# Optimization experiments

Measured on AMD Instinct MI355X. Metric: run time of the kernel, lower is better.

Reference implementation:

```python
import jax, jax.numpy as jnp
import numpy as np

DELTA = 1.0 / 1024.0  # init kwarg `delta`


def _lin_init(key, out_f, in_f):
    k1, k2 = jax.random.split(key)
    s = 1.0 / np.sqrt(in_f)
    w = jax.random.uniform(k1, (out_f, in_f), minval=-s, maxval=s, dtype=jnp.float32)
    b = jax.random.uniform(k2, (out_f,), minval=-s, maxval=s, dtype=jnp.float32)
    return w, b


def setup_inputs() -> dict:
    key = jax.random.key(0)
    B, S, C, H, T = 262144, 64, 8, 64, 1024  # batch, state_dim, control_dim, rnn hidden, seq len
    ks = jax.random.split(key, 12)
    t = jax.random.uniform(ks[0], (B, 1), dtype=jnp.float32)            # in [0,1) -> t_u in [0,T)
    x = jax.random.normal(ks[1], (B, S), dtype=jnp.float32)
    u = jax.random.normal(ks[2], (T, C), dtype=jnp.float32)
    i2h_w, i2h_b = _lin_init(ks[3], H, C + H)
    h2o_w, h2o_b = _lin_init(ks[4], S, C + H)
    xw1, xb1 = _lin_init(ks[5], 20, 1 + S)
    xw2, xb2 = _lin_init(ks[6], 20, 20)
    xw3, xb3 = _lin_init(ks[7], S, 20)
    uw1, ub1 = _lin_init(ks[8], 20, 1 + S)
    uw2, ub2 = _lin_init(ks[9], 20, 20)
    uw3, ub3 = _lin_init(ks[10], S, 20)
    cw, cb = _lin_init(ks[11], S, 2 * S)
    return {"t": t, "x": x, "u": u,
            "i2h_w": i2h_w, "i2h_b": i2h_b, "h2o_w": h2o_w, "h2o_b": h2o_b,
            "xw1": xw1, "xb1": xb1, "xw2": xw2, "xb2": xb2, "xw3": xw3, "xb3": xb3,
            "uw1": uw1, "ub1": ub1, "uw2": uw2, "ub2": ub2, "uw3": uw3, "ub3": ub3,
            "cw": cw, "cb": cb}


def _mlp(z, w1, b1, w2, b2, w3, b3):
    h = jax.nn.sigmoid(z @ w1.T + b1)
    h = jax.nn.sigmoid(h @ w2.T + b2)
    return h @ w3.T + b3


def reference(t, x, u, i2h_w, i2h_b, h2o_w, h2o_b,
              xw1, xb1, xw2, xb2, xw3, xb3,
              uw1, ub1, uw2, ub2, uw3, ub3, cw, cb):
    # state branch: x_dnn([t, x])
    state_part = _mlp(jnp.concatenate([t, x], axis=1), xw1, xb1, xw2, xb2, xw3, xb3)

    # sequential tanh-RNN over the control sequence (hidden starts at zero)
    hsz = i2h_w.shape[0]

    def step(h, u_k):
        j = jnp.concatenate([u_k, h])                 # (C+H,)
        h_new = jnp.tanh(j @ i2h_w.T + i2h_b)         # (H,)
        out = jnp.tanh(j @ h2o_w.T + h2o_b)           # (S,)
        return h_new, out

    h0 = jnp.zeros((hsz,), dtype=u.dtype)
    _, u_rnn_out = jax.lax.scan(step, h0, u)          # (T, S)

    # gather encoded controls per query time
    t_u = jnp.floor(t / DELTA).astype(jnp.int32).squeeze(-1)  # (B,)
    encoded_controls = u_rnn_out[t_u]                 # (B, S)

    control_part = _mlp(jnp.concatenate([t, encoded_controls], axis=1),
                        uw1, ub1, uw2, ub2, uw3, ub3)

    stacked = jax.nn.sigmoid(jnp.concatenate([state_part, control_part], axis=1))  # (B, 2S)
    return stacked @ cw.T + cb
```

## Files before the change

kernel.cpp:

```cpp
#include <hip/hip_runtime.h>
#include <hip/hip_bf16.h>

#define T_SEQ 1024
#define CHUNK 64
#define NCHUNK 16

__device__ __forceinline__ float fast_sigmoid(float x) {
    return 1.0f / (1.0f + __expf(-x));
}
__device__ __forceinline__ float fast_tanh(float x) {
    float e = __expf(2.0f * x);
    return 1.0f - 2.0f / (e + 1.0f);
}

__device__ __forceinline__ float quad_sum(float x) {
    int y1 = __builtin_amdgcn_mov_dpp(__float_as_int(x), 0xB1, 0xF, 0xF, true);
    float s1 = x + __int_as_float(y1);
    int y2 = __builtin_amdgcn_mov_dpp(__float_as_int(s1), 0x4E, 0xF, 0xF, true);
    return s1 + __int_as_float(y2);
}

#define P_SW1 0
#define P_SB1 1360
#define P_SW2 1380
#define P_SB2 1780
#define P_UW1 1800
#define P_UB1 3160
#define P_UW2 3180
#define P_UB2 3580
#define P_XW3 3600
#define P_XB3 4880
#define P_UW3 4944
#define P_UB3 6224
#define P_CWT 6288
#define P_CB  14480
#define P_TOT 14544

__global__ __launch_bounds__(256) void k_prep(
    const float* __restrict__ u,
    const float* __restrict__ i2h_w, const float* __restrict__ i2h_b,
    const float* __restrict__ h2o_w, const float* __restrict__ h2o_b,
    const float* __restrict__ xw1, const float* __restrict__ uw1,
    const float* __restrict__ xw2, const float* __restrict__ uw2,
    const float* __restrict__ xw3, const float* __restrict__ uw3,
    const float* __restrict__ cw,
    const float* __restrict__ xb1, const float* __restrict__ xb2,
    const float* __restrict__ ub1, const float* __restrict__ ub2,
    const float* __restrict__ xb3, const float* __restrict__ ub3,
    const float* __restrict__ cb,
    float* __restrict__ pre_t, float* __restrict__ pre_o,
    float* __restrict__ wp) {
    const int bid = blockIdx.x, tid = threadIdx.x;
    if (bid < 256) {
        int idx = bid * 256 + tid;
        int k = idx >> 6, i = idx & 63;
        float a = i2h_b[i], b = h2o_b[i];
#pragma unroll
        for (int c = 0; c < 8; ++c) {
            float uv = u[k * 8 + c];
            a += uv * i2h_w[i * 72 + c];
            b += uv * h2o_w[i * 72 + c];
        }
        pre_t[i * 1024 + k] = a;
        pre_o[idx] = b;
        return;
    }
    int i = (bid - 256) * 256 + tid;
    if (i >= P_TOT) return;
    float v = 0.0f;
    if (i < 1360) {
        int o = i / 68, c = i - o * 68;
        if (c == 0) v = xw1[o * 65];
        else if (c >= 4) v = xw1[o * 65 + c - 3];
    } else if (i < 1380) v = xb1[i - 1360];
    else if (i < 1780) v = xw2[i - 1380];
    else if (i < 1800) v = xb2[i - 1780];
    else if (i < 3160) {
        int j = i - 1800; int o = j / 68, c = j - o * 68;
        if (c == 0) v = uw1[o * 65];
        else if (c >= 4) v = uw1[o * 65 + c - 3];
    } else if (i < 3180) v = ub1[i - 3160];
    else if (i < 3580) v = uw2[i - 3180];
    else if (i < 3600) v = ub2[i - 3580];
    else if (i < 4880) v = xw3[i - 3600];
    else if (i < 4944) v = xb3[i - 4880];
    else if (i < 6224) v = uw3[i - 4944];
    else if (i < 6288) v = ub3[i - 6224];
    else if (i < 14480) {
        int j = i - 6288; int row = j >> 6, s = j & 63;
        v = cw[s * 128 + row];
    }
    else v = cb[i - 14480];
    wp[i] = v;
}

__global__ __launch_bounds__(256) void k_rnn_out(
    const float* __restrict__ h2o_w,
    const float* __restrict__ pre_o,
    const float* __restrict__ hseq,
    float* __restrict__ uout) {
    const int tid = threadIdx.x;
    const int sub = tid >> 6, i = tid & 63;
    const int k = blockIdx.x * 4 + sub;
    __shared__ float hk[4][64];
    hk[sub][i] = hseq[k * 64 + i];
    __syncthreads();
    float acc = pre_o[k * 64 + i];
    const float4* h4 = reinterpret_cast<const float4*>(hk[sub]);
#pragma unroll
    for (int v = 0; v < 16; ++v) {
        float4 hv = h4[v];
        acc += h2o_w[i * 72 + 8 + 4*v+0] * hv.x + h2o_w[i * 72 + 8 + 4*v+1] * hv.y
             + h2o_w[i * 72 + 8 + 4*v+2] * hv.z + h2o_w[i * 72 + 8 + 4*v+3] * hv.w;
    }
    uout[k * 64 + i] = fast_tanh(acc);
}

template <int OW1, int OB1, int OW2, int OB2>
__device__ __forceinline__ void mlp20(const float* __restrict__ sm,
                                      float tval, const float4* z, float* h2) {
    float h1[20];
#pragma unroll 4
    for (int o = 0; o < 20; ++o) {
        const int ro = OW1 + o * 68;
        float a = sm[OB1 + o] + tval * sm[ro];
        const float4* wr = reinterpret_cast<const float4*>(&sm[ro + 4]);
#pragma unroll
        for (int v = 0; v < 16; ++v) {
            float4 w4 = wr[v];
            a += z[v].x * w4.x + z[v].y * w4.y + z[v].z * w4.z + z[v].w * w4.w;
        }
        h1[o] = fast_sigmoid(a);
    }
#pragma unroll 4
    for (int o = 0; o < 20; ++o) {
        float a = sm[OB2 + o];
        const float4* wr = reinterpret_cast<const float4*>(&sm[OW2 + o * 20]);
#pragma unroll
        for (int v = 0; v < 5; ++v) {
            float4 w4 = wr[v];
            a += h1[4*v+0]*w4.x + h1[4*v+1]*w4.y + h1[4*v+2]*w4.z + h1[4*v+3]*w4.w;
        }
        h2[o] = fast_sigmoid(a);
    }
}

template <int OW3, int OB3, int OCWT>
__device__ __forceinline__ void final64(const float* __restrict__ sm,
                                        const float* h2, float* oacc) {
#pragma unroll 2
    for (int o = 0; o < 64; ++o) {
        float a = sm[OB3 + o];
        const float4* wr = reinterpret_cast<const float4*>(&sm[OW3 + o * 20]);
#pragma unroll
        for (int v = 0; v < 5; ++v) {
            float4 w4 = wr[v];
            a += h2[4*v+0]*w4.x + h2[4*v+1]*w4.y + h2[4*v+2]*w4.z + h2[4*v+3]*w4.w;
        }
        float s = fast_sigmoid(a);
        const float4* cr = reinterpret_cast<const float4*>(&sm[OCWT + o * 64]);
#pragma unroll
        for (int v = 0; v < 16; ++v) {
            float4 c4 = cr[v];
            oacc[4*v+0] += s * c4.x; oacc[4*v+1] += s * c4.y;
            oacc[4*v+2] += s * c4.z; oacc[4*v+3] += s * c4.w;
        }
    }
}

#define SMEMF_MAIN 14544

__global__ __launch_bounds__(256) void k_main(
    const float* __restrict__ t_in, const float* __restrict__ x_in,
    const float* __restrict__ i2h_w,
    const float* __restrict__ pre_t,
    const float* __restrict__ wp,
    float* __restrict__ hseq, float* __restrict__ out) {
    __shared__ float smem[SMEMF_MAIN];
    const int tid = threadIdx.x;
    const int bid = blockIdx.x;

    if (bid == 0) {
        __builtin_amdgcn_s_setprio(3);
        float* hs = smem;
        const int lane = tid & 63;
        const int wv = tid >> 6;
        const int t = lane >> 2;
        const int j = lane & 3;
        const int o = 16 * wv + t;

        float wih[16];
#pragma unroll
        for (int jj = 0; jj < 16; ++jj) wih[jj] = i2h_w[o * 72 + 8 + 16 * jj / 16 * 0 + 16 * j + jj];
#pragma unroll
        for (int jj = 0; jj < 16; ++jj) wih[jj] = i2h_w[o * 72 + 8 + 16 * j + jj];

        if (tid < 64) hs[tid] = 0.0f;
        __syncthreads();
        const float4* h4 = reinterpret_cast<const float4*>(hs);

        for (int c = 0; c < NCHUNK; ++c) {
            float preg[64];
            {
                const float4* pt = reinterpret_cast<const float4*>(pre_t + o * 1024 + c * 64);
#pragma unroll
                for (int q = 0; q < 16; ++q) {
                    float4 p = pt[q];
                    preg[4*q+0] = p.x; preg[4*q+1] = p.y;
                    preg[4*q+2] = p.z; preg[4*q+3] = p.w;
                }
            }
#pragma unroll
            for (int s = 0; s < CHUNK; ++s) {
                const float4* hb = h4 + s * 16 + 4 * j;
                float4 b0 = hb[0], b1 = hb[1], b2 = hb[2], b3 = hb[3];
                float a0 = wih[ 0]*b0.x + wih[ 1]*b0.y + wih[ 2]*b0.z + wih[ 3]*b0.w;
                float a1 = wih[ 4]*b1.x + wih[ 5]*b1.y + wih[ 6]*b1.z + wih[ 7]*b1.w;
                float a2 = wih[ 8]*b2.x + wih[ 9]*b2.y + wih[10]*b2.z + wih[11]*b2.w;
                float a3 = wih[12]*b3.x + wih[13]*b3.y + wih[14]*b3.z + wih[15]*b3.w;
                float tot = quad_sum((a0 + a1) + (a2 + a3));
                float hn = fast_tanh(tot + preg[s]);
                if (j == 0) hs[(s + 1) * 64 + o] = hn;
                __syncthreads();
            }
            {
                const float4* hsrc = reinterpret_cast<const float4*>(hs);
                float4* hdst = reinterpret_cast<float4*>(hseq + c * 4096);
#pragma unroll
                for (int q = 0; q < 4; ++q) hdst[tid * 4 + q] = hsrc[tid * 4 + q];
            }
            __syncthreads();
            if (tid < 64) hs[tid] = hs[4096 + tid];
            __syncthreads();
        }
        return;
    }

    {
        float4* s4 = reinterpret_cast<float4*>(smem);
        const float4* w4 = reinterpret_cast<const float4*>(wp);
        for (int idx = tid; idx < P_TOT / 4; idx += 256) s4[idx] = w4[idx];
    }
    __syncthreads();

    const int r = (bid - 1) * 256 + tid;
    float tval = t_in[r];
    float4 z[16];
    const float4* xp = reinterpret_cast<const float4*>(x_in + (size_t)r * 64);
#pragma unroll
    for (int v = 0; v < 16; ++v) z[v] = xp[v];

    float h2[20];
    mlp20<P_SW1, P_SB1, P_SW2, P_SB2>(smem, tval, z, h2);

    float oacc[64];
    {
        const float4* cbp = reinterpret_cast<const float4*>(&smem[P_CB]);
#pragma unroll
        for (int v = 0; v < 16; ++v) {
            float4 c4 = cbp[v];
            oacc[4*v+0] = c4.x; oacc[4*v+1] = c4.y;
            oacc[4*v+2] = c4.z; oacc[4*v+3] = c4.w;
        }
    }
    final64<P_XW3, P_XB3, P_CWT>(smem, h2, oacc);

    float4* op = reinterpret_cast<float4*>(out + (size_t)r * 64);
#pragma unroll
    for (int v = 0; v < 16; ++v) {
        float4 f;
        f.x = oacc[4*v+0]; f.y = oacc[4*v+1];
        f.z = oacc[4*v+2]; f.w = oacc[4*v+3];
        op[v] = f;
    }
}

__global__ __launch_bounds__(256) void k_ctrl(
    const float* __restrict__ t_in, const float* __restrict__ uo,
    const float* __restrict__ wp, float* __restrict__ out) {
    __shared__ float sm[P_TOT];
    const int tid = threadIdx.x;
    {
        float4* s4 = reinterpret_cast<float4*>(sm);
        const float4* w4 = reinterpret_cast<const float4*>(wp);
        for (int idx = tid; idx < P_TOT / 4; idx += 256) s4[idx] = w4[idx];
    }
    __syncthreads();

    const int r = blockIdx.x * 256 + tid;
    float tval = t_in[r];
    int ti = min((int)(tval * 1024.0f), 1023);
    float4 z[16];
    const float4* ep = reinterpret_cast<const float4*>(uo + ti * 64);
#pragma unroll
    for (int v = 0; v < 16; ++v) z[v] = ep[v];

    float h2[20];
    mlp20<P_UW1, P_UB1, P_UW2, P_UB2>(sm, tval, z, h2);

    float oacc[64];
    float4* op = reinterpret_cast<float4*>(out + (size_t)r * 64);
#pragma unroll
    for (int v = 0; v < 16; ++v) {
        float4 f = op[v];
        oacc[4*v+0] = f.x; oacc[4*v+1] = f.y;
        oacc[4*v+2] = f.z; oacc[4*v+3] = f.w;
    }
    final64<P_UW3, P_UB3, P_CWT + 64 * 64>(sm, h2, oacc);
#pragma unroll
    for (int v = 0; v < 16; ++v) {
        float4 f;
        f.x = oacc[4*v+0]; f.y = oacc[4*v+1];
        f.z = oacc[4*v+2]; f.w = oacc[4*v+3];
        op[v] = f;
    }
}

extern "C" void kernel_launch(void* const* d_in, const int* in_sizes, int n_in,
                              void* d_out, int out_size, void* d_ws, size_t ws_size,
                              hipStream_t stream) {
    const float* t     = (const float*)d_in[0];
    const float* x     = (const float*)d_in[1];
    const float* u     = (const float*)d_in[2];
    const float* i2h_w = (const float*)d_in[3];
    const float* i2h_b = (const float*)d_in[4];
    const float* h2o_w = (const float*)d_in[5];
    const float* h2o_b = (const float*)d_in[6];
    const float* xw1 = (const float*)d_in[7];  const float* xb1 = (const float*)d_in[8];
    const float* xw2 = (const float*)d_in[9];  const float* xb2 = (const float*)d_in[10];
    const float* xw3 = (const float*)d_in[11]; const float* xb3 = (const float*)d_in[12];
    const float* uw1 = (const float*)d_in[13]; const float* ub1 = (const float*)d_in[14];
    const float* uw2 = (const float*)d_in[15]; const float* ub2 = (const float*)d_in[16];
    const float* uw3 = (const float*)d_in[17]; const float* ub3 = (const float*)d_in[18];
    const float* cw  = (const float*)d_in[19]; const float* cb  = (const float*)d_in[20];
    float* out = (float*)d_out;

    float* ws = (float*)d_ws;
    float* pre_t = ws;
    float* uo    = ws;
    float* pre_o = ws + 65536;
    float* hseq  = ws + 131072;
    float* wp    = ws + 196608;

    int Bv = in_sizes[0];

    hipLaunchKernelGGL(k_prep, dim3(256 + (P_TOT + 255) / 256), dim3(256), 0, stream,
                       u, i2h_w, i2h_b, h2o_w, h2o_b,
                       xw1, uw1, xw2, uw2, xw3, uw3, cw,
                       xb1, xb2, ub1, ub2, xb3, ub3, cb,
                       pre_t, pre_o, wp);
    hipLaunchKernelGGL(k_main, dim3(1 + Bv / 256), dim3(256), 0, stream,
                       t, x, i2h_w, pre_t, wp, hseq, out);
    hipLaunchKernelGGL(k_rnn_out, dim3(T_SEQ / 4), dim3(256), 0, stream,
                       h2o_w, pre_o, hseq, uo);
    hipLaunchKernelGGL(k_ctrl, dim3(Bv / 256), dim3(256), 0, stream,
                       t, uo, wp, out);
}
```

Before: 312.5 us.

## Fuse RNN output and control MLP into persistent kernel with chunk flags

Replaces the separate rnn_out and control kernels with one persistent 512-block kernel. Block 0 runs the recurrence and signals each finished chunk through a flag. Block 1 computes the RNN outputs per chunk and raises a second flag. The remaining blocks run the state MLP over their rows, bucket those rows by time chunk, and run the control MLP as soon as the needed chunk is published. This is meant to hide the serial RNN behind the batch work and drop two kernel launches. It relies on all 512 blocks being co-resident and spin-waiting, which risks deadlock or stalls, and it adds extra output read-modify-write traffic.

```diff
diff --git a/kernel.cpp b/kernel.cpp
--- a/kernel.cpp
+++ b/kernel.cpp
@@ -94,28 +94,6 @@
     wp[i] = v;
 }
 
-__global__ __launch_bounds__(256) void k_rnn_out(
-    const float* __restrict__ h2o_w,
-    const float* __restrict__ pre_o,
-    const float* __restrict__ hseq,
-    float* __restrict__ uout) {
-    const int tid = threadIdx.x;
-    const int sub = tid >> 6, i = tid & 63;
-    const int k = blockIdx.x * 4 + sub;
-    __shared__ float hk[4][64];
-    hk[sub][i] = hseq[k * 64 + i];
-    __syncthreads();
-    float acc = pre_o[k * 64 + i];
-    const float4* h4 = reinterpret_cast<const float4*>(hk[sub]);
-#pragma unroll
-    for (int v = 0; v < 16; ++v) {
-        float4 hv = h4[v];
-        acc += h2o_w[i * 72 + 8 + 4*v+0] * hv.x + h2o_w[i * 72 + 8 + 4*v+1] * hv.y
-             + h2o_w[i * 72 + 8 + 4*v+2] * hv.z + h2o_w[i * 72 + 8 + 4*v+3] * hv.w;
-    }
-    uout[k * 64 + i] = fast_tanh(acc);
-}
-
 template <int OW1, int OB1, int OW2, int OB2>
 __device__ __forceinline__ void mlp20(const float* __restrict__ sm,
                                       float tval, const float4* z, float* h2) {
@@ -168,15 +146,17 @@
     }
 }
 
-#define SMEMF_MAIN 14544
-
-__global__ __launch_bounds__(256) void k_main(
+#define SMEMF_OV 15104
+
+__global__ __launch_bounds__(256) void k_main_ov(
     const float* __restrict__ t_in, const float* __restrict__ x_in,
-    const float* __restrict__ i2h_w,
-    const float* __restrict__ pre_t,
+    const float* __restrict__ i2h_w, const float* __restrict__ h2o_w,
+    const float* __restrict__ pre_t, const float* __restrict__ pre_o,
     const float* __restrict__ wp,
-    float* __restrict__ hseq, float* __restrict__ out) {
-    __shared__ float smem[SMEMF_MAIN];
+    float* __restrict__ hseq, float* __restrict__ uo,
+    int* __restrict__ flag1, int* __restrict__ flag2,
+    float* __restrict__ out) {
+    __shared__ float smem[SMEMF_OV];
     const int tid = threadIdx.x;
     const int bid = blockIdx.x;
 
@@ -190,8 +170,6 @@
         const int o = 16 * wv + t;
 
         float wih[16];
-#pragma unroll
-        for (int jj = 0; jj < 16; ++jj) wih[jj] = i2h_w[o * 72 + 8 + 16 * jj / 16 * 0 + 16 * j + jj];
 #pragma unroll
         for (int jj = 0; jj < 16; ++jj) wih[jj] = i2h_w[o * 72 + 8 + 16 * j + jj];
 
@@ -230,6 +208,218 @@
                 for (int q = 0; q < 4; ++q) hdst[tid * 4 + q] = hsrc[tid * 4 + q];
             }
             __syncthreads();
+            if (tid == 0)
+                __hip_atomic_store(&flag1[c], 1, __ATOMIC_RELEASE, __HIP_MEMORY_SCOPE_AGENT);
+            if (tid < 64) hs[tid] = hs[4096 + tid];
+            __syncthreads();
+        }
+        return;
+    }
+
+    if (bid == 1) {
+        float* hk = smem;
+        const int lane = tid & 63;
+        const int wv = tid >> 6;
+        float who[64];
+#pragma unroll
+        for (int m = 0; m < 64; ++m) who[m] = h2o_w[lane * 72 + 8 + m];
+
+        for (int c = 0; c < NCHUNK; ++c) {
+            while (__hip_atomic_load(&flag1[c], __ATOMIC_ACQUIRE, __HIP_MEMORY_SCOPE_AGENT) == 0)
+                __builtin_amdgcn_s_sleep(8);
+            {
+                const float4* hg = reinterpret_cast<const float4*>(hseq + c * 4096);
+                float4* hd = reinterpret_cast<float4*>(hk);
+#pragma unroll
+                for (int q = 0; q < 4; ++q) hd[tid * 4 + q] = hg[tid * 4 + q];
+            }
+            __syncthreads();
+            float preg[16];
+#pragma unroll
+            for (int rr = 0; rr < 16; ++rr)
+                preg[rr] = pre_o[(c * 64 + wv * 16 + rr) * 64 + lane];
+#pragma unroll 2
+            for (int rr = 0; rr < 16; ++rr) {
+                const float4* hv4 = reinterpret_cast<const float4*>(hk + (wv * 16 + rr) * 64);
+                float acc = preg[rr];
+#pragma unroll
+                for (int v = 0; v < 16; ++v) {
+                    float4 hv = hv4[v];
+                    acc += who[4*v+0]*hv.x + who[4*v+1]*hv.y
+                         + who[4*v+2]*hv.z + who[4*v+3]*hv.w;
+                }
+                uo[(c * 64 + wv * 16 + rr) * 64 + lane] = fast_tanh(acc);
+            }
+            __syncthreads();
+            if (tid == 0)
+                __hip_atomic_store(&flag2[c], 1, __ATOMIC_RELEASE, __HIP_MEMORY_SCOPE_AGENT);
+        }
+        return;
+    }
+
+    {
+        float4* s4 = reinterpret_cast<float4*>(smem);
+        const float4* w4 = reinterpret_cast<const float4*>(wp);
+        for (int idx = tid; idx < P_TOT / 4; idx += 256) s4[idx] = w4[idx];
+    }
+    __syncthreads();
+
+    const int ib = bid - 2;
+    const int r0 = ib * 514 + min(ib, 4);
+    const int count = 514 + (ib < 4 ? 1 : 0);
+    const int r1 = r0 + count;
+
+    for (int r = r0 + tid; r < r1; r += 256) {
+        float tval = t_in[r];
+        float4 z[16];
+        const float4* xp = reinterpret_cast<const float4*>(x_in + (size_t)r * 64);
+#pragma unroll
+        for (int v = 0; v < 16; ++v) z[v] = xp[v];
+        float h2[20];
+        mlp20<P_SW1, P_SB1, P_SW2, P_SB2>(smem, tval, z, h2);
+        float oacc[64];
+        {
+            const float4* cbp = reinterpret_cast<const float4*>(&smem[P_CB]);
+#pragma unroll
+            for (int v = 0; v < 16; ++v) {
+                float4 c4 = cbp[v];
+                oacc[4*v+0] = c4.x; oacc[4*v+1] = c4.y;
+                oacc[4*v+2] = c4.z; oacc[4*v+3] = c4.w;
+            }
+        }
+        final64<P_XW3, P_XB3, P_CWT>(smem, h2, oacc);
+        float4* op = reinterpret_cast<float4*>(out + (size_t)r * 64);
+#pragma unroll
+        for (int v = 0; v < 16; ++v) {
+            float4 f;
+            f.x = oacc[4*v+0]; f.y = oacc[4*v+1];
+            f.z = oacc[4*v+2]; f.w = oacc[4*v+3];
+            op[v] = f;
+        }
+    }
+
+    int* order = (int*)&smem[P_TOT];
+    int* hist  = (int*)&smem[P_TOT + 520];
+    int* basep = (int*)&smem[P_TOT + 536];
+    if (tid < 16) hist[tid] = 0;
+    __syncthreads();
+    for (int r = r0 + tid; r < r1; r += 256) {
+        int ti = min((int)(t_in[r] * 1024.0f), 1023);
+        atomicAdd(&hist[ti >> 6], 1);
+    }
+    __syncthreads();
+    if (tid == 0) {
+        int acc = 0;
+#pragma unroll
+        for (int k = 0; k < 16; ++k) { basep[k] = acc; acc += hist[k]; hist[k] = basep[k]; }
+    }
+    __syncthreads();
+    for (int r = r0 + tid; r < r1; r += 256) {
+        int ti = min((int)(t_in[r] * 1024.0f), 1023);
+        int pos = atomicAdd(&hist[ti >> 6], 1);
+        order[pos] = r;
+    }
+    __syncthreads();
+
+    const int niter = (count + 255) >> 8;
+    for (int it = 0; it < niter; ++it) {
+        int p = tid + it * 256;
+        bool act = p < count;
+        int row = act ? order[p] : r0;
+        float tval = t_in[row];
+        int ti = min((int)(tval * 1024.0f), 1023);
+        int m = act ? (ti >> 6) : 0;
+#pragma unroll
+        for (int off = 32; off >= 1; off >>= 1) m = max(m, __shfl_xor(m, off));
+        while (__hip_atomic_load(&flag2[m], __ATOMIC_ACQUIRE, __HIP_MEMORY_SCOPE_AGENT) == 0)
+            __builtin_amdgcn_s_sleep(8);
+        if (act) {
+            float4 z[16];
+            const float4* ep = reinterpret_cast<const float4*>(uo + ti * 64);
+#pragma unroll
+            for (int v = 0; v < 16; ++v) z[v] = ep[v];
+            float h2[20];
+            mlp20<P_UW1, P_UB1, P_UW2, P_UB2>(smem, tval, z, h2);
+            float oacc[64];
+            float4* op = reinterpret_cast<float4*>(out + (size_t)row * 64);
+#pragma unroll
+            for (int v = 0; v < 16; ++v) {
+                float4 f = op[v];
+                oacc[4*v+0] = f.x; oacc[4*v+1] = f.y;
+                oacc[4*v+2] = f.z; oacc[4*v+3] = f.w;
+            }
+            final64<P_UW3, P_UB3, P_CWT + 64 * 64>(smem, h2, oacc);
+#pragma unroll
+            for (int v = 0; v < 16; ++v) {
+                float4 f;
+                f.x = oacc[4*v+0]; f.y = oacc[4*v+1];
+                f.z = oacc[4*v+2]; f.w = oacc[4*v+3];
+                op[v] = f;
+            }
+        }
+    }
+}
+
+#define SMEMF_MAIN 14544
+
+__global__ __launch_bounds__(256) void k_main(
+    const float* __restrict__ t_in, const float* __restrict__ x_in,
+    const float* __restrict__ i2h_w,
+    const float* __restrict__ pre_t,
+    const float* __restrict__ wp,
+    float* __restrict__ hseq, float* __restrict__ out) {
+    __shared__ float smem[SMEMF_MAIN];
+    const int tid = threadIdx.x;
+    const int bid = blockIdx.x;
+
+    if (bid == 0) {
+        __builtin_amdgcn_s_setprio(3);
+        float* hs = smem;
+        const int lane = tid & 63;
+        const int wv = tid >> 6;
+        const int t = lane >> 2;
+        const int j = lane & 3;
+        const int o = 16 * wv + t;
+
+        float wih[16];
+#pragma unroll
+        for (int jj = 0; jj < 16; ++jj) wih[jj] = i2h_w[o * 72 + 8 + 16 * j + jj];
+
+        if (tid < 64) hs[tid] = 0.0f;
+        __syncthreads();
+        const float4* h4 = reinterpret_cast<const float4*>(hs);
+
+        for (int c = 0; c < NCHUNK; ++c) {
+            float preg[64];
+            {
+                const float4* pt = reinterpret_cast<const float4*>(pre_t + o * 1024 + c * 64);
+#pragma unroll
+                for (int q = 0; q < 16; ++q) {
+                    float4 p = pt[q];
+                    preg[4*q+0] = p.x; preg[4*q+1] = p.y;
+                    preg[4*q+2] = p.z; preg[4*q+3] = p.w;
+                }
+            }
+#pragma unroll
+            for (int s = 0; s < CHUNK; ++s) {
+                const float4* hb = h4 + s * 16 + 4 * j;
+                float4 b0 = hb[0], b1 = hb[1], b2 = hb[2], b3 = hb[3];
+                float a0 = wih[ 0]*b0.x + wih[ 1]*b0.y + wih[ 2]*b0.z + wih[ 3]*b0.w;
+                float a1 = wih[ 4]*b1.x + wih[ 5]*b1.y + wih[ 6]*b1.z + wih[ 7]*b1.w;
+                float a2 = wih[ 8]*b2.x + wih[ 9]*b2.y + wih[10]*b2.z + wih[11]*b2.w;
+                float a3 = wih[12]*b3.x + wih[13]*b3.y + wih[14]*b3.z + wih[15]*b3.w;
+                float tot = quad_sum((a0 + a1) + (a2 + a3));
+                float hn = fast_tanh(tot + preg[s]);
+                if (j == 0) hs[(s + 1) * 64 + o] = hn;
+                __syncthreads();
+            }
+            {
+                const float4* hsrc = reinterpret_cast<const float4*>(hs);
+                float4* hdst = reinterpret_cast<float4*>(hseq + c * 4096);
+#pragma unroll
+                for (int q = 0; q < 4; ++q) hdst[tid * 4 + q] = hsrc[tid * 4 + q];
+            }
+            __syncthreads();
             if (tid < 64) hs[tid] = hs[4096 + tid];
             __syncthreads();
         }
@@ -273,6 +463,28 @@
         f.z = oacc[4*v+2]; f.w = oacc[4*v+3];
         op[v] = f;
     }
+}
+
+__global__ __launch_bounds__(256) void k_rnn_out(
+    const float* __restrict__ h2o_w,
+    const float* __restrict__ pre_o,
+    const float* __restrict__ hseq,
+    float* __restrict__ uout) {
+    const int tid = threadIdx.x;
+    const int sub = tid >> 6, i = tid & 63;
+    const int k = blockIdx.x * 4 + sub;
+    __shared__ float hk[4][64];
+    hk[sub][i] = hseq[k * 64 + i];
+    __syncthreads();
+    float acc = pre_o[k * 64 + i];
+    const float4* h4 = reinterpret_cast<const float4*>(hk[sub]);
+#pragma unroll
+    for (int v = 0; v < 16; ++v) {
+        float4 hv = h4[v];
+        acc += h2o_w[i * 72 + 8 + 4*v+0] * hv.x + h2o_w[i * 72 + 8 + 4*v+1] * hv.y
+             + h2o_w[i * 72 + 8 + 4*v+2] * hv.z + h2o_w[i * 72 + 8 + 4*v+3] * hv.w;
+    }
+    uout[k * 64 + i] = fast_tanh(acc);
 }
 
 __global__ __launch_bounds__(256) void k_ctrl(
@@ -336,23 +548,44 @@
     float* out = (float*)d_out;
 
     float* ws = (float*)d_ws;
-    float* pre_t = ws;
-    float* uo    = ws;
-    float* pre_o = ws + 65536;
-    float* hseq  = ws + 131072;
-    float* wp    = ws + 196608;
-
     int Bv = in_sizes[0];
 
-    hipLaunchKernelGGL(k_prep, dim3(256 + (P_TOT + 255) / 256), dim3(256), 0, stream,
-                       u, i2h_w, i2h_b, h2o_w, h2o_b,
-                       xw1, uw1, xw2, uw2, xw3, uw3, cw,
-                       xb1, xb2, ub1, ub2, xb3, ub3, cb,
-                       pre_t, pre_o, wp);
-    hipLaunchKernelGGL(k_main, dim3(1 + Bv / 256), dim3(256), 0, stream,
-                       t, x, i2h_w, pre_t, wp, hseq, out);
-    hipLaunchKernelGGL(k_rnn_out, dim3(T_SEQ / 4), dim3(256), 0, stream,
-                       h2o_w, pre_o, hseq, uo);
-    hipLaunchKernelGGL(k_ctrl, dim3(Bv / 256), dim3(256), 0, stream,
-                       t, uo, wp, out);
-}
+    const size_t need = (size_t)(276720) * sizeof(float);
+    if (ws_size >= need) {
+        float* pre_t = ws;
+        float* pre_o = ws + 65536;
+        float* hseq  = ws + 131072;
+        float* uo    = ws + 196608;
+        float* wp    = ws + 262144;
+        int*   flag1 = (int*)(ws + 276688);
+        int*   flag2 = flag1 + 16;
+
+        hipLaunchKernelGGL(k_prep, dim3(256 + (P_TOT + 255) / 256), dim3(256), 0, stream,
+                           u, i2h_w, i2h_b, h2o_w, h2o_b,
+                           xw1, uw1, xw2, uw2, xw3, uw3, cw,
+                           xb1, xb2, ub1, ub2, xb3, ub3, cb,
+                           pre_t, pre_o, wp);
+        hipMemsetAsync(flag1, 0, 32 * sizeof(int), stream);
+        hipLaunchKernelGGL(k_main_ov, dim3(512), dim3(256), 0, stream,
+                           t, x, i2h_w, h2o_w, pre_t, pre_o, wp,
+                           hseq, uo, flag1, flag2, out);
+    } else {
+        float* pre_t = ws;
+        float* uo    = ws;
+        float* pre_o = ws + 65536;
+        float* hseq  = ws + 131072;
+        float* wp    = ws + 196608;
+
+        hipLaunchKernelGGL(k_prep, dim3(256 + (P_TOT + 255) / 256), dim3(256), 0, stream,
+                           u, i2h_w, i2h_b, h2o_w, h2o_b,
+                           xw1, uw1, xw2, uw2, xw3, uw3, cw,
+                           xb1, xb2, ub1, ub2, xb3, ub3, cb,
+                           pre_t, pre_o, wp);
+        hipLaunchKernelGGL(k_main, dim3(1 + Bv / 256), dim3(256), 0, stream,
+                           t, x, i2h_w, pre_t, wp, hseq, out);
+        hipLaunchKernelGGL(k_rnn_out, dim3(T_SEQ / 4), dim3(256), 0, stream,
+                           h2o_w, pre_o, hseq, uo);
+        hipLaunchKernelGGL(k_ctrl, dim3(Bv / 256), dim3(256), 0, stream,
+                           t, uo, wp, out);
+    }
+}
```

New measurement: 366.2 us. 1.17x slower.
